# Optimization experiments

Measured on AMD Instinct MI355X. Metric: run time of the kernel, lower is better.

Reference implementation:

```python
import jax, jax.numpy as jnp
import numpy as np

N, H, F, E, K = 4096, 512, 2048, 8, 2  # tokens, hidden, ffn(=4H), experts, top_k


def setup_inputs() -> dict:
    key = jax.random.key(0)
    ks = jax.random.split(key, 7)
    def w(k, shape, fan_in):
        return jax.random.normal(k, shape, dtype=jnp.float32) * (fan_in ** -0.5)
    return {
        "x": jax.random.normal(ks[0], (N, H), dtype=jnp.float32),
        "W_in": w(ks[1], (H, H), H),          # input_proj.weight  [out,in]
        "W_router": w(ks[2], (E, H), H),      # router.gate.weight [E,H]
        "W_gate": w(ks[3], (E, F, H), H),     # per-expert gate_proj.weight
        "W_up": w(ks[4], (E, F, H), H),       # per-expert up_proj.weight
        "W_down": w(ks[5], (E, H, F), F),     # per-expert down_proj.weight
        "W_out": w(ks[6], (H, H), H),         # output_proj.weight
    }


def reference(x, W_in, W_router, W_gate, W_up, W_down, W_out):
    h = x @ W_in.T                                  # [N,H] input_proj
    logits = h @ W_router.T                         # [N,E]
    # route_mode='balanced' and world_size==1 -> expert_bias is None
    probs = jax.nn.softmax(logits, axis=-1)
    top_w, top_i = jax.lax.top_k(probs, K)          # [N,K]
    top_w = jax.nn.softmax(top_w, axis=-1)          # renormalize over top-k

    # per-token combine weight for each expert: [N,E]
    onehot = jax.nn.one_hot(top_i, E, dtype=h.dtype)      # [N,K,E]
    combine_w = jnp.einsum('nk,nke->ne', top_w, onehot)

    def expert(wg, wu, wd):
        # SwiGLU FFN: down( silu(gate(h)) * up(h) )
        return (jax.nn.silu(h @ wg.T) * (h @ wu.T)) @ wd.T  # [N,H]

    expert_out = jax.vmap(expert)(W_gate, W_up, W_down)     # [E,N,H]
    combined = jnp.einsum('ne,enh->nh', combine_w, expert_out)
    return combined @ W_out.T                                # output_proj
```

## Files before the change

### kernel.cpp

```cpp
#include <hip/hip_runtime.h>

typedef unsigned short u16;
typedef unsigned int u32;
typedef short bf16x8 __attribute__((ext_vector_type(8)));
typedef float f32x4 __attribute__((ext_vector_type(4)));

#define AS1 __attribute__((address_space(1)))
#define AS3 __attribute__((address_space(3)))

#define NTOK 4096
#define HDIM 512
#define FDIM 2048
#define NEXP 8
#define NASSIGN (NTOK * 2)
#define NPAD (NASSIGN + NEXP * 128)
#define RBMAX 128

__device__ __forceinline__ void g2l16(const void* g, void* l) {
  __builtin_amdgcn_global_load_lds((const AS1 u32*)g, (AS3 u32*)l, 16, 0, 0);
}
__device__ __forceinline__ u16 f2bf(float f) {
  u32 u = __float_as_uint(f);
  u = (u + 0x7FFFu + ((u >> 16) & 1u)) >> 16;
  return (u16)u;
}
__device__ __forceinline__ float bf2f(u16 h) { return __uint_as_float(((u32)h) << 16); }

#define WAITV6() asm volatile("s_waitcnt vmcnt(6)" ::: "memory")
#define WAITV4() asm volatile("s_waitcnt vmcnt(4)" ::: "memory")
#define WAITV0() asm volatile("s_waitcnt vmcnt(0)" ::: "memory")
#define BAR() __builtin_amdgcn_s_barrier()
#define VMBAR() do { WAITV0(); BAR(); } while (0)

__global__ __launch_bounds__(256) void cvtall_kernel(
    const float* __restrict__ x, const float* __restrict__ Wi, const float* __restrict__ Wo,
    const float* __restrict__ Wg, const float* __restrict__ Wu, const float* __restrict__ Wd,
    u16* __restrict__ xb, u16* __restrict__ Wib, u16* __restrict__ Wob,
    u16* __restrict__ Wgb, u16* __restrict__ Wub, u16* __restrict__ Wdb) {
  const int gid = blockIdx.x * 256 + threadIdx.x;
  const int S = 6784 * 256;
#pragma unroll
  for (int k = 0; k < 4; ++k) {
    const int i = gid + k * S;
    const float* s; u16* d; int o;
    if (i < 524288) { s = x; d = xb; o = i; }
    else if (i < 589824) { s = Wi; d = Wib; o = i - 524288; }
    else if (i < 655360) { s = Wo; d = Wob; o = i - 589824; }
    else if (i < 2752512) { s = Wg; d = Wgb; o = i - 655360; }
    else if (i < 4849664) { s = Wu; d = Wub; o = i - 2752512; }
    else { s = Wd; d = Wdb; o = i - 4849664; }
    const float4 v = ((const float4*)s)[o];
    ushort4 t; t.x = f2bf(v.x); t.y = f2bf(v.y); t.z = f2bf(v.z); t.w = f2bf(v.w);
    ((ushort4*)d)[o] = t;
  }
}

__global__ __launch_bounds__(256) void wreff_kernel(
    const float* __restrict__ Wr, const float* __restrict__ Wi, double* __restrict__ wre) {
  const int t = blockIdx.x * 256 + threadIdx.x;
  const int e = t >> 9, k = t & 511;
  const float* wr = Wr + e * HDIM;
  double a = 0.0;
  for (int j = 0; j < HDIM; j += 8) {
#pragma unroll
    for (int u = 0; u < 8; ++u) a += (double)wr[j + u] * (double)Wi[(j + u) * HDIM + k];
  }
  wre[t] = a;
}

__global__ __launch_bounds__(256) void router_kernel(
    const float* __restrict__ x, const double* __restrict__ wre,
    int* __restrict__ idx, float* __restrict__ wts) {
  __shared__ double lw[NEXP * HDIM];
  for (int i = threadIdx.x; i < NEXP * HDIM; i += 256) lw[i] = wre[i];
  __syncthreads();
  const int n = blockIdx.x * 256 + threadIdx.x;
  const float* xr = x + (size_t)n * HDIM;
  double acc[NEXP] = {};
  for (int k4 = 0; k4 < HDIM / 4; ++k4) {
    const float4 xv = ((const float4*)xr)[k4];
    const float xc[4] = {xv.x, xv.y, xv.z, xv.w};
#pragma unroll
    for (int c = 0; c < 4; ++c) {
      const double xd = (double)xc[c];
#pragma unroll
      for (int e = 0; e < NEXP; ++e) acc[e] += xd * lw[e * HDIM + k4 * 4 + c];
    }
  }
  double mx = acc[0];
#pragma unroll
  for (int e = 1; e < NEXP; ++e) mx = acc[e] > mx ? acc[e] : mx;
  double p[NEXP], se = 0.0;
#pragma unroll
  for (int e = 0; e < NEXP; ++e) { p[e] = exp(acc[e] - mx); se += p[e]; }
  const double inv = 1.0 / se;
#pragma unroll
  for (int e = 0; e < NEXP; ++e) p[e] *= inv;
  int i0 = 0; double b0 = p[0];
#pragma unroll
  for (int e = 1; e < NEXP; ++e) if (p[e] > b0) { b0 = p[e]; i0 = e; }
  int i1 = -1; double b1 = -1.0;
#pragma unroll
  for (int e = 0; e < NEXP; ++e) if (e != i0 && p[e] > b1) { b1 = p[e]; i1 = e; }
  const double e0 = exp(b0), e1 = exp(b1);
  idx[2 * n] = i0; idx[2 * n + 1] = i1;
  wts[2 * n] = (float)(e0 / (e0 + e1));
  wts[2 * n + 1] = (float)(e1 / (e0 + e1));
}

__global__ void assign_kernel(const int* __restrict__ idx, int* __restrict__ tok,
                              int* __restrict__ pos, int* __restrict__ rbe,
                              int* __restrict__ rbp, int* __restrict__ nrb) {
  __shared__ int cnt[NEXP], cur[NEXP];
  const int tid = threadIdx.x;
  if (tid < NEXP) cnt[tid] = 0;
  __syncthreads();
  for (int a = tid; a < NASSIGN; a += 256) atomicAdd(&cnt[idx[a]], 1);
  __syncthreads();
  if (tid == 0) {
    int o = 0, n = 0;
    for (int e = 0; e < NEXP; ++e) {
      cur[e] = o;
      const int nb = (cnt[e] + 127) >> 7;
      for (int i = 0; i < nb; ++i) { rbe[n] = e; rbp[n] = o + i * 128; ++n; }
      o += nb * 128;
    }
    nrb[0] = n;
  }
  __syncthreads();
  for (int p = tid; p < NPAD; p += 256) tok[p] = 0;
  __syncthreads();
  for (int a = tid; a < NASSIGN; a += 256) {
    const int e = idx[a];
    const int q = atomicAdd(&cur[e], 1);
    tok[q] = a >> 1;
    pos[a] = q;
  }
}

template <int SB, int NT>
__device__ __forceinline__ void gemm128_body(
    const u16* __restrict__ A, const u16* __restrict__ B, void* __restrict__ C,
    int m0, int n0, int N, int K, u16* sm, int tid) {
  u16 *lA0 = sm, *lA1 = sm + 8192, *lB0 = sm + 16384, *lB1 = sm + 24576;
  const int w = tid >> 6, l = tid & 63;
  const int wm = (w >> 2) * 64, wn = (w & 3) * 32;
  const int lm = l & 15, lk = (l >> 4) * 8, xr = (l & 7) << 3;
  const int sr = l >> 3, sc = ((l & 7) ^ sr) * 8;
  const u16* As = A + (size_t)(m0 + w * 8 + sr) * K + sc;
  const u16* Bs = B + (size_t)(n0 + w * 8 + sr) * K + sc;
  f32x4 acc[4][2] = {};
  auto STG = [&](u16* dA, u16* dB, int kt) {
    g2l16(As + kt, dA + w * 512);
    g2l16(As + (size_t)64 * K + kt, dA + 4096 + w * 512);
    g2l16(Bs + kt, dB + w * 512);
    g2l16(Bs + (size_t)64 * K + kt, dB + 4096 + w * 512);
  };
  auto CMP = [&](const u16* a_, const u16* b_) {
#pragma unroll
    for (int kk = 0; kk < 2; ++kk) {
      const int ko = (kk * 32 + lk) ^ xr;
      bf16x8 af[4], bf[2];
#pragma unroll
      for (int i = 0; i < 4; ++i) af[i] = *(const bf16x8*)(a_ + (wm + i * 16 + lm) * 64 + ko);
#pragma unroll
      for (int j = 0; j < 2; ++j) bf[j] = *(const bf16x8*)(b_ + (wn + j * 16 + lm) * 64 + ko);
#pragma unroll
      for (int i = 0; i < 4; ++i)
#pragma unroll
        for (int j = 0; j < 2; ++j)
          acc[i][j] = __builtin_amdgcn_mfma_f32_16x16x32_bf16(af[i], bf[j], acc[i][j], 0, 0, 0);
    }
  };
  STG(lA0, lB0, 0);
  VMBAR();
  for (int t = 0; t < NT; t += 2) {
    if (t + 1 < NT) STG(lA1, lB1, (t + 1) * 64);
    CMP(lA0, lB0);
    VMBAR();
    if (t + 2 < NT) STG(lA0, lB0, (t + 2) * 64);
    CMP(lA1, lB1);
    VMBAR();
  }
  const int cr = (l >> 4) * 4, cc = lm;
#pragma unroll
  for (int i = 0; i < 4; ++i)
#pragma unroll
    for (int j = 0; j < 2; ++j)
#pragma unroll
      for (int r = 0; r < 4; ++r) {
        const size_t o = (size_t)(m0 + wm + i * 16 + cr + r) * N + n0 + wn + j * 16 + cc;
        if (SB) ((u16*)C)[o] = f2bf(acc[i][j][r]);
        else ((float*)C)[o] = acc[i][j][r];
      }
}

__global__ __launch_bounds__(512, 2) void ingemm_kernel(
    const u16* __restrict__ xb, const u16* __restrict__ Wib, u16* __restrict__ hb) {
  __shared__ __align__(16) u16 sm[32768];
  gemm128_body<1, 8>(xb, Wib, hb, blockIdx.y * 128, blockIdx.x * 128, HDIM, HDIM, sm, threadIdx.x);
}

__global__ __launch_bounds__(512, 2) void outgemm_kernel(
    const u16* __restrict__ cb, const u16* __restrict__ Wob, float* __restrict__ out) {
  __shared__ __align__(16) u16 sm[32768];
  gemm128_body<0, 8>(cb, Wob, out, blockIdx.y * 128, blockIdx.x * 128, HDIM, HDIM, sm, threadIdx.x);
}

__global__ __launch_bounds__(512, 2) void gateup_kernel(
    const u16* __restrict__ hb, const u16* __restrict__ Wg, const u16* __restrict__ Wu,
    u16* __restrict__ act, const int* __restrict__ tok, const int* __restrict__ rbe,
    const int* __restrict__ rbp, const int* __restrict__ nrb) {
  const int rb = blockIdx.y;
  if (rb >= nrb[0]) return;
  __shared__ __align__(16) u16 sm[73728];
  const int e = rbe[rb], p0 = rbp[rb], n0 = blockIdx.x * 128;
  const int tid = threadIdx.x, w = tid >> 6, l = tid & 63;
  const int wm = (w >> 2) * 64, wn = (w & 3) * 32;
  const int lm = l & 15, lk = (l >> 4) * 8, xr = (l & 7) << 3;
  const int sr = l >> 3, sc = ((l & 7) ^ sr) * 8;
  const u16* A0 = hb + (size_t)tok[p0 + w * 8 + sr] * HDIM + sc;
  const u16* A1 = hb + (size_t)tok[p0 + 64 + w * 8 + sr] * HDIM + sc;
  const u16* G0 = Wg + (size_t)e * FDIM * HDIM + (size_t)(n0 + w * 8 + sr) * HDIM + sc;
  const u16* G1 = G0 + (size_t)64 * HDIM;
  const u16* U0 = Wu + (size_t)e * FDIM * HDIM + (size_t)(n0 + w * 8 + sr) * HDIM + sc;
  const u16* U1 = U0 + (size_t)64 * HDIM;
  f32x4 ag[4][2] = {}, au[4][2] = {};
  auto STG = [&](int b, int kt) {
    u16* d = sm + b * 24576;
    g2l16(A0 + kt, d + w * 512);
    g2l16(A1 + kt, d + 4096 + w * 512);
    g2l16(G0 + kt, d + 8192 + w * 512);
    g2l16(G1 + kt, d + 12288 + w * 512);
    g2l16(U0 + kt, d + 16384 + w * 512);
    g2l16(U1 + kt, d + 20480 + w * 512);
  };
  auto CMP = [&](int b) {
    const u16* a_ = sm + b * 24576;
    const u16* g_ = a_ + 8192;
    const u16* u_ = a_ + 16384;
#pragma unroll
    for (int kk = 0; kk < 2; ++kk) {
      const int ko = (kk * 32 + lk) ^ xr;
      bf16x8 af[4], gf[2], uf[2];
#pragma unroll
      for (int i = 0; i < 4; ++i) af[i] = *(const bf16x8*)(a_ + (wm + i * 16 + lm) * 64 + ko);
#pragma unroll
      for (int j = 0; j < 2; ++j) {
        gf[j] = *(const bf16x8*)(g_ + (wn + j * 16 + lm) * 64 + ko);
        uf[j] = *(const bf16x8*)(u_ + (wn + j * 16 + lm) * 64 + ko);
      }
#pragma unroll
      for (int i = 0; i < 4; ++i)
#pragma unroll
        for (int j = 0; j < 2; ++j) {
          ag[i][j] = __builtin_amdgcn_mfma_f32_16x16x32_bf16(af[i], gf[j], ag[i][j], 0, 0, 0);
          au[i][j] = __builtin_amdgcn_mfma_f32_16x16x32_bf16(af[i], uf[j], au[i][j], 0, 0, 0);
        }
    }
  };
  STG(0, 0); STG(1, 64);
  WAITV6(); BAR();
#pragma unroll
  for (int t = 0; t < 8; ++t) {
    if (t + 2 < 8) STG((t + 2) % 3, (t + 2) * 64);
    CMP(t % 3);
    if (t + 2 < 8) WAITV6(); else WAITV0();
    BAR();
  }
  const int cr = (l >> 4) * 4, cc = lm;
#pragma unroll
  for (int i = 0; i < 4; ++i)
#pragma unroll
    for (int j = 0; j < 2; ++j)
#pragma unroll
      for (int r = 0; r < 4; ++r) {
        const float g = ag[i][j][r], u = au[i][j][r];
        const float s = g / (1.0f + __expf(-g));
        act[(size_t)(p0 + wm + i * 16 + cr + r) * FDIM + n0 + wn + j * 16 + cc] = f2bf(s * u);
      }
}

__global__ __launch_bounds__(512, 2) void down_kernel(
    const u16* __restrict__ act, const u16* __restrict__ Wd, u16* __restrict__ dwn,
    const int* __restrict__ rbe, const int* __restrict__ rbp, const int* __restrict__ nrb) {
  const int rb = blockIdx.y;
  if (rb >= nrb[0]) return;
  __shared__ __align__(16) u16 sm[49152];
  const int e = rbe[rb], p0 = rbp[rb], n0 = blockIdx.x * 128;
  const int tid = threadIdx.x, w = tid >> 6, l = tid & 63;
  const int g = w >> 2;
  const int wm = ((w >> 1) & 1) * 64, wn = (w & 1) * 64;
  const int lm = l & 15, lk = (l >> 4) * 8, xr = (l & 7) << 3;
  const int ko = (g * 32 + lk) ^ xr;
  const int sr = l >> 3, sc = ((l & 7) ^ sr) * 8;
  const u16* As = act + (size_t)(p0 + w * 8 + sr) * FDIM + sc;
  const u16* Bs = Wd + (size_t)e * HDIM * FDIM + (size_t)(n0 + w * 8 + sr) * FDIM + sc;
  f32x4 acc[4][4] = {};
  auto STG = [&](int b, int kt) {
    u16* d = sm + b * 16384;
    g2l16(As + kt, d + w * 512);
    g2l16(As + (size_t)64 * FDIM + kt, d + 4096 + w * 512);
    g2l16(Bs + kt, d + 8192 + w * 512);
    g2l16(Bs + (size_t)64 * FDIM + kt, d + 12288 + w * 512);
  };
  auto CMP = [&](int b) {
    const u16* a_ = sm + b * 16384;
    const u16* b_ = a_ + 8192;
    bf16x8 af[4], bf[4];
#pragma unroll
    for (int i = 0; i < 4; ++i) af[i] = *(const bf16x8*)(a_ + (wm + i * 16 + lm) * 64 + ko);
#pragma unroll
    for (int j = 0; j < 4; ++j) bf[j] = *(const bf16x8*)(b_ + (wn + j * 16 + lm) * 64 + ko);
#pragma unroll
    for (int i = 0; i < 4; ++i)
#pragma unroll
      for (int j = 0; j < 4; ++j)
        acc[i][j] = __builtin_amdgcn_mfma_f32_16x16x32_bf16(af[i], bf[j], acc[i][j], 0, 0, 0);
  };
  STG(0, 0); STG(1, 64);
  WAITV4(); BAR();
#pragma unroll
  for (int t = 0; t < 32; ++t) {
    if (t + 2 < 32) STG((t + 2) % 3, (t + 2) * 64);
    CMP(t % 3);
    if (t + 2 < 32) WAITV4(); else WAITV0();
    BAR();
  }
  asm volatile("s_waitcnt lgkmcnt(0)" ::: "memory");
  __builtin_amdgcn_sched_barrier(0);
  BAR();
  float* red = (float*)sm;
  if (g == 1) {
#pragma unroll
    for (int i = 0; i < 4; ++i)
#pragma unroll
      for (int j = 0; j < 4; ++j)
        *(f32x4*)&red[(w & 3) * 4096 + (i * 4 + j) * 256 + l * 4] = acc[i][j];
  }
  BAR();
  if (g == 0) {
    const int cr = (l >> 4) * 4, cc = lm;
#pragma unroll
    for (int i = 0; i < 4; ++i)
#pragma unroll
      for (int j = 0; j < 4; ++j) {
        const f32x4 o = *(const f32x4*)&red[w * 4096 + (i * 4 + j) * 256 + l * 4];
        const f32x4 s = acc[i][j] + o;
#pragma unroll
        for (int r = 0; r < 4; ++r)
          dwn[(size_t)(p0 + wm + i * 16 + cr + r) * HDIM + n0 + wn + j * 16 + cc] = f2bf(s[r]);
      }
  }
}

__global__ void combine_kernel(const u16* __restrict__ dwn, const int* __restrict__ pos,
                               const float* __restrict__ wts, u16* __restrict__ cb) {
  const int n = blockIdx.x, t = threadIdx.x;
  const int p0 = pos[2 * n], p1 = pos[2 * n + 1];
  const float w0 = wts[2 * n], w1 = wts[2 * n + 1];
  const ushort4 a = ((const ushort4*)(dwn + (size_t)p0 * HDIM))[t];
  const ushort4 b = ((const ushort4*)(dwn + (size_t)p1 * HDIM))[t];
  ushort4 o;
  o.x = f2bf(w0 * bf2f(a.x) + w1 * bf2f(b.x));
  o.y = f2bf(w0 * bf2f(a.y) + w1 * bf2f(b.y));
  o.z = f2bf(w0 * bf2f(a.z) + w1 * bf2f(b.z));
  o.w = f2bf(w0 * bf2f(a.w) + w1 * bf2f(b.w));
  ((ushort4*)(cb + (size_t)n * HDIM))[t] = o;
}

extern "C" void kernel_launch(void* const* d_in, const int* in_sizes, int n_in,
                              void* d_out, int out_size, void* d_ws, size_t ws_size,
                              hipStream_t stream) {
  const float* x  = (const float*)d_in[0];
  const float* Wi = (const float*)d_in[1];
  const float* Wr = (const float*)d_in[2];
  const float* Wg = (const float*)d_in[3];
  const float* Wu = (const float*)d_in[4];
  const float* Wd = (const float*)d_in[5];
  const float* Wo = (const float*)d_in[6];
  float* out = (float*)d_out;

  char* ws = (char*)d_ws;
  size_t off = 0;
  auto alloc = [&](size_t bytes) -> void* {
    off = (off + 255) & ~(size_t)255;
    void* p = ws + off;
    off += bytes;
    return p;
  };
  u16* xb  = (u16*)alloc((size_t)NTOK * HDIM * 2);
  u16* hb  = (u16*)alloc((size_t)NTOK * HDIM * 2);
  u16* cb  = (u16*)alloc((size_t)NTOK * HDIM * 2);
  u16* Wib = (u16*)alloc((size_t)HDIM * HDIM * 2);
  u16* Wob = (u16*)alloc((size_t)HDIM * HDIM * 2);
  u16* Wgb = (u16*)alloc((size_t)NEXP * FDIM * HDIM * 2);
  u16* Wub = (u16*)alloc((size_t)NEXP * FDIM * HDIM * 2);
  u16* Wdb = (u16*)alloc((size_t)NEXP * HDIM * FDIM * 2);
  u16* actb = (u16*)alloc((size_t)NPAD * FDIM * 2);
  u16* dwn = (u16*)alloc((size_t)NPAD * HDIM * 2);
  double* wre = (double*)alloc((size_t)NEXP * HDIM * 8);
  int* idx = (int*)alloc((size_t)NASSIGN * 4);
  float* wts = (float*)alloc((size_t)NASSIGN * 4);
  int* tok = (int*)alloc((size_t)NPAD * 4);
  int* pos = (int*)alloc((size_t)NASSIGN * 4);
  int* rbe = (int*)alloc((size_t)RBMAX * 4);
  int* rbp = (int*)alloc((size_t)RBMAX * 4);
  int* nrb = (int*)alloc(256);

  cvtall_kernel<<<6784, 256, 0, stream>>>(x, Wi, Wo, Wg, Wu, Wd, xb, Wib, Wob, Wgb, Wub, Wdb);
  wreff_kernel<<<16, 256, 0, stream>>>(Wr, Wi, wre);
  router_kernel<<<16, 256, 0, stream>>>(x, wre, idx, wts);
  assign_kernel<<<1, 256, 0, stream>>>(idx, tok, pos, rbe, rbp, nrb);
  ingemm_kernel<<<dim3(4, 32), 512, 0, stream>>>(xb, Wib, hb);
  gateup_kernel<<<dim3(16, 72), 512, 0, stream>>>(hb, Wgb, Wub, actb, tok, rbe, rbp, nrb);
  down_kernel<<<dim3(4, 72), 512, 0, stream>>>(actb, Wdb, dwn, rbe, rbp, nrb);
  combine_kernel<<<NTOK, 128, 0, stream>>>(dwn, pos, wts, cb);
  outgemm_kernel<<<dim3(4, 32), 512, 0, stream>>>(cb, Wob, out);
}
```

Before: 218.2 us.

## Retile MoE gate/up to 256-row blocks, simplify down GEMM, fuse router-weight prep

Result: slower. 226.7 us (+3.9%).

```diff
diff --git a/kernel.cpp b/kernel.cpp
--- a/kernel.cpp
+++ b/kernel.cpp
@@ -13,7 +13,7 @@
 #define FDIM 2048
 #define NEXP 8
 #define NASSIGN (NTOK * 2)
-#define NPAD (NASSIGN + NEXP * 128)
+#define NPAD2 (NASSIGN + NEXP * 256)
 #define RBMAX 128
 
 __device__ __forceinline__ void g2l16(const void* g, void* l) {
@@ -26,7 +26,6 @@
 }
 __device__ __forceinline__ float bf2f(u16 h) { return __uint_as_float(((u32)h) << 16); }
 
-#define WAITV6() asm volatile("s_waitcnt vmcnt(6)" ::: "memory")
 #define WAITV4() asm volatile("s_waitcnt vmcnt(4)" ::: "memory")
 #define WAITV0() asm volatile("s_waitcnt vmcnt(0)" ::: "memory")
 #define BAR() __builtin_amdgcn_s_barrier()
@@ -35,46 +34,48 @@
 __global__ __launch_bounds__(256) void cvtall_kernel(
     const float* __restrict__ x, const float* __restrict__ Wi, const float* __restrict__ Wo,
     const float* __restrict__ Wg, const float* __restrict__ Wu, const float* __restrict__ Wd,
+    const float* __restrict__ Wr,
     u16* __restrict__ xb, u16* __restrict__ Wib, u16* __restrict__ Wob,
-    u16* __restrict__ Wgb, u16* __restrict__ Wub, u16* __restrict__ Wdb) {
-  const int gid = blockIdx.x * 256 + threadIdx.x;
-  const int S = 6784 * 256;
-#pragma unroll
-  for (int k = 0; k < 4; ++k) {
-    const int i = gid + k * S;
-    const float* s; u16* d; int o;
-    if (i < 524288) { s = x; d = xb; o = i; }
-    else if (i < 589824) { s = Wi; d = Wib; o = i - 524288; }
-    else if (i < 655360) { s = Wo; d = Wob; o = i - 589824; }
-    else if (i < 2752512) { s = Wg; d = Wgb; o = i - 655360; }
-    else if (i < 4849664) { s = Wu; d = Wub; o = i - 2752512; }
-    else { s = Wd; d = Wdb; o = i - 4849664; }
-    const float4 v = ((const float4*)s)[o];
-    ushort4 t; t.x = f2bf(v.x); t.y = f2bf(v.y); t.z = f2bf(v.z); t.w = f2bf(v.w);
-    ((ushort4*)d)[o] = t;
-  }
-}
-
-__global__ __launch_bounds__(256) void wreff_kernel(
-    const float* __restrict__ Wr, const float* __restrict__ Wi, double* __restrict__ wre) {
-  const int t = blockIdx.x * 256 + threadIdx.x;
-  const int e = t >> 9, k = t & 511;
-  const float* wr = Wr + e * HDIM;
-  double a = 0.0;
-  for (int j = 0; j < HDIM; j += 8) {
-#pragma unroll
-    for (int u = 0; u < 8; ++u) a += (double)wr[j + u] * (double)Wi[(j + u) * HDIM + k];
-  }
-  wre[t] = a;
-}
-
-__global__ __launch_bounds__(256) void router_kernel(
+    u16* __restrict__ Wgb, u16* __restrict__ Wub, u16* __restrict__ Wdb,
+    double* __restrict__ wre) {
+  const int b = blockIdx.x, tid = threadIdx.x;
+  if (b < 6784) {
+    const int gid = b * 256 + tid;
+    const int S = 6784 * 256;
+#pragma unroll
+    for (int k = 0; k < 4; ++k) {
+      const int i = gid + k * S;
+      const float* s; u16* d; int o;
+      if (i < 524288) { s = x; d = xb; o = i; }
+      else if (i < 589824) { s = Wi; d = Wib; o = i - 524288; }
+      else if (i < 655360) { s = Wo; d = Wob; o = i - 589824; }
+      else if (i < 2752512) { s = Wg; d = Wgb; o = i - 655360; }
+      else if (i < 4849664) { s = Wu; d = Wub; o = i - 2752512; }
+      else { s = Wd; d = Wdb; o = i - 4849664; }
+      const float4 v = ((const float4*)s)[o];
+      ushort4 t; t.x = f2bf(v.x); t.y = f2bf(v.y); t.z = f2bf(v.z); t.w = f2bf(v.w);
+      ((ushort4*)d)[o] = t;
+    }
+  } else {
+    const int t = (b - 6784) * 256 + tid;
+    const int e = t >> 9, k = t & 511;
+    const float* wr = Wr + e * HDIM;
+    double a = 0.0;
+    for (int j = 0; j < HDIM; j += 8) {
+#pragma unroll
+      for (int u = 0; u < 8; ++u) a += (double)wr[j + u] * (double)Wi[(j + u) * HDIM + k];
+    }
+    wre[t] = a;
+  }
+}
+
+__global__ __launch_bounds__(128) void router_kernel(
     const float* __restrict__ x, const double* __restrict__ wre,
     int* __restrict__ idx, float* __restrict__ wts) {
   __shared__ double lw[NEXP * HDIM];
-  for (int i = threadIdx.x; i < NEXP * HDIM; i += 256) lw[i] = wre[i];
+  for (int i = threadIdx.x; i < NEXP * HDIM; i += 128) lw[i] = wre[i];
   __syncthreads();
-  const int n = blockIdx.x * 256 + threadIdx.x;
+  const int n = blockIdx.x * 128 + threadIdx.x;
   const float* xr = x + (size_t)n * HDIM;
   double acc[NEXP] = {};
   for (int k4 = 0; k4 < HDIM / 4; ++k4) {
@@ -109,8 +110,9 @@
 }
 
 __global__ void assign_kernel(const int* __restrict__ idx, int* __restrict__ tok,
-                              int* __restrict__ pos, int* __restrict__ rbe,
-                              int* __restrict__ rbp, int* __restrict__ nrb) {
+                              int* __restrict__ pos, int* __restrict__ rbe2,
+                              int* __restrict__ rbp2, int* __restrict__ rbe1,
+                              int* __restrict__ rbp1, int* __restrict__ nrb) {
   __shared__ int cnt[NEXP], cur[NEXP];
   const int tid = threadIdx.x;
   if (tid < NEXP) cnt[tid] = 0;
@@ -118,17 +120,19 @@
   for (int a = tid; a < NASSIGN; a += 256) atomicAdd(&cnt[idx[a]], 1);
   __syncthreads();
   if (tid == 0) {
-    int o = 0, n = 0;
+    int o = 0, n2 = 0, n1 = 0;
     for (int e = 0; e < NEXP; ++e) {
       cur[e] = o;
-      const int nb = (cnt[e] + 127) >> 7;
-      for (int i = 0; i < nb; ++i) { rbe[n] = e; rbp[n] = o + i * 128; ++n; }
-      o += nb * 128;
-    }
-    nrb[0] = n;
+      const int nb2 = (cnt[e] + 255) >> 8;
+      const int nb1 = (cnt[e] + 127) >> 7;
+      for (int i = 0; i < nb2; ++i) { rbe2[n2] = e; rbp2[n2] = o + i * 256; ++n2; }
+      for (int i = 0; i < nb1; ++i) { rbe1[n1] = e; rbp1[n1] = o + i * 128; ++n1; }
+      o += nb2 * 256;
+    }
+    nrb[0] = n2; nrb[1] = n1;
   }
   __syncthreads();
-  for (int p = tid; p < NPAD; p += 256) tok[p] = 0;
+  for (int p = tid; p < NPAD2; p += 256) tok[p] = 0;
   __syncthreads();
   for (int a = tid; a < NASSIGN; a += 256) {
     const int e = idx[a];
@@ -209,149 +213,130 @@
 
 __global__ __launch_bounds__(512, 2) void gateup_kernel(
     const u16* __restrict__ hb, const u16* __restrict__ Wg, const u16* __restrict__ Wu,
-    u16* __restrict__ act, const int* __restrict__ tok, const int* __restrict__ rbe,
-    const int* __restrict__ rbp, const int* __restrict__ nrb) {
+    u16* __restrict__ act, const int* __restrict__ tok, const int* __restrict__ rbe2,
+    const int* __restrict__ rbp2, const int* __restrict__ nrb) {
   const int rb = blockIdx.y;
   if (rb >= nrb[0]) return;
-  __shared__ __align__(16) u16 sm[73728];
-  const int e = rbe[rb], p0 = rbp[rb], n0 = blockIdx.x * 128;
+  __shared__ __align__(16) u16 sm[49152];
+  const int e = rbe2[rb], p0 = rbp2[rb], n0 = blockIdx.x * 128;
   const int tid = threadIdx.x, w = tid >> 6, l = tid & 63;
-  const int wm = (w >> 2) * 64, wn = (w & 3) * 32;
-  const int lm = l & 15, lk = (l >> 4) * 8, xr = (l & 7) << 3;
-  const int sr = l >> 3, sc = ((l & 7) ^ sr) * 8;
-  const u16* A0 = hb + (size_t)tok[p0 + w * 8 + sr] * HDIM + sc;
-  const u16* A1 = hb + (size_t)tok[p0 + 64 + w * 8 + sr] * HDIM + sc;
-  const u16* G0 = Wg + (size_t)e * FDIM * HDIM + (size_t)(n0 + w * 8 + sr) * HDIM + sc;
-  const u16* G1 = G0 + (size_t)64 * HDIM;
-  const u16* U0 = Wu + (size_t)e * FDIM * HDIM + (size_t)(n0 + w * 8 + sr) * HDIM + sc;
-  const u16* U1 = U0 + (size_t)64 * HDIM;
-  f32x4 ag[4][2] = {}, au[4][2] = {};
-  auto STG = [&](int b, int kt) {
-    u16* d = sm + b * 24576;
-    g2l16(A0 + kt, d + w * 512);
-    g2l16(A1 + kt, d + 4096 + w * 512);
-    g2l16(G0 + kt, d + 8192 + w * 512);
-    g2l16(G1 + kt, d + 12288 + w * 512);
-    g2l16(U0 + kt, d + 16384 + w * 512);
-    g2l16(U1 + kt, d + 20480 + w * 512);
+  const int lrow = l >> 2;
+  const int scb = ((l & 3) ^ ((lrow >> 1) & 3)) * 8;
+  const int rm = (w >> 2) * 128, cg = (w & 3) * 32;
+  const int lm = l & 15;
+  const int koe = ((l >> 4) ^ ((l >> 1) & 3)) << 3;
+  const u16* As0 = hb + (size_t)tok[p0 + (w * 2 + 0) * 16 + lrow] * HDIM + scb;
+  const u16* As1 = hb + (size_t)tok[p0 + (w * 2 + 1) * 16 + lrow] * HDIM + scb;
+  const u16* Gs = Wg + (size_t)e * FDIM * HDIM + (size_t)(n0 + w * 16 + lrow) * HDIM + scb;
+  const u16* Us = Wu + (size_t)e * FDIM * HDIM + (size_t)(n0 + w * 16 + lrow) * HDIM + scb;
+  f32x4 ag[8][2] = {}, au[8][2] = {};
+  auto STG = [&](int b, int t) {
+    u16* base = sm + b * 16384;
+    const int kt = t * 32;
+    g2l16(As0 + kt, base + (w * 2 + 0) * 512);
+    g2l16(As1 + kt, base + (w * 2 + 1) * 512);
+    g2l16(Gs + kt, base + 8192 + w * 512);
+    g2l16(Us + kt, base + 12288 + w * 512);
   };
   auto CMP = [&](int b) {
-    const u16* a_ = sm + b * 24576;
+    const u16* a_ = sm + b * 16384;
     const u16* g_ = a_ + 8192;
-    const u16* u_ = a_ + 16384;
-#pragma unroll
-    for (int kk = 0; kk < 2; ++kk) {
-      const int ko = (kk * 32 + lk) ^ xr;
-      bf16x8 af[4], gf[2], uf[2];
-#pragma unroll
-      for (int i = 0; i < 4; ++i) af[i] = *(const bf16x8*)(a_ + (wm + i * 16 + lm) * 64 + ko);
+    const u16* u_ = a_ + 12288;
+    bf16x8 gf[2], uf[2];
+#pragma unroll
+    for (int j = 0; j < 2; ++j) {
+      gf[j] = *(const bf16x8*)(g_ + (cg + j * 16 + lm) * 32 + koe);
+      uf[j] = *(const bf16x8*)(u_ + (cg + j * 16 + lm) * 32 + koe);
+    }
+#pragma unroll
+    for (int i = 0; i < 8; ++i) {
+      const bf16x8 af = *(const bf16x8*)(a_ + (rm + i * 16 + lm) * 32 + koe);
 #pragma unroll
       for (int j = 0; j < 2; ++j) {
-        gf[j] = *(const bf16x8*)(g_ + (wn + j * 16 + lm) * 64 + ko);
-        uf[j] = *(const bf16x8*)(u_ + (wn + j * 16 + lm) * 64 + ko);
+        ag[i][j] = __builtin_amdgcn_mfma_f32_16x16x32_bf16(af, gf[j], ag[i][j], 0, 0, 0);
+        au[i][j] = __builtin_amdgcn_mfma_f32_16x16x32_bf16(af, uf[j], au[i][j], 0, 0, 0);
       }
-#pragma unroll
-      for (int i = 0; i < 4; ++i)
-#pragma unroll
-        for (int j = 0; j < 2; ++j) {
-          ag[i][j] = __builtin_amdgcn_mfma_f32_16x16x32_bf16(af[i], gf[j], ag[i][j], 0, 0, 0);
-          au[i][j] = __builtin_amdgcn_mfma_f32_16x16x32_bf16(af[i], uf[j], au[i][j], 0, 0, 0);
-        }
-    }
-  };
-  STG(0, 0); STG(1, 64);
-  WAITV6(); BAR();
-#pragma unroll
-  for (int t = 0; t < 8; ++t) {
-    if (t + 2 < 8) STG((t + 2) % 3, (t + 2) * 64);
+    }
+  };
+  STG(0, 0); STG(1, 1);
+  WAITV4(); BAR();
+#pragma unroll
+  for (int t = 0; t < 16; ++t) {
+    if (t + 2 < 16) STG((t + 2) % 3, t + 2);
     CMP(t % 3);
-    if (t + 2 < 8) WAITV6(); else WAITV0();
+    if (t + 2 < 16) { WAITV4(); } else { WAITV0(); }
     BAR();
   }
   const int cr = (l >> 4) * 4, cc = lm;
 #pragma unroll
-  for (int i = 0; i < 4; ++i)
+  for (int i = 0; i < 8; ++i)
 #pragma unroll
     for (int j = 0; j < 2; ++j)
 #pragma unroll
       for (int r = 0; r < 4; ++r) {
         const float g = ag[i][j][r], u = au[i][j][r];
         const float s = g / (1.0f + __expf(-g));
-        act[(size_t)(p0 + wm + i * 16 + cr + r) * FDIM + n0 + wn + j * 16 + cc] = f2bf(s * u);
+        act[(size_t)(p0 + rm + i * 16 + cr + r) * FDIM + n0 + cg + j * 16 + cc] = f2bf(s * u);
       }
 }
 
-__global__ __launch_bounds__(512, 2) void down_kernel(
+__global__ __launch_bounds__(256, 3) void down_kernel(
     const u16* __restrict__ act, const u16* __restrict__ Wd, u16* __restrict__ dwn,
-    const int* __restrict__ rbe, const int* __restrict__ rbp, const int* __restrict__ nrb) {
+    const int* __restrict__ rbe1, const int* __restrict__ rbp1, const int* __restrict__ nrb) {
   const int rb = blockIdx.y;
-  if (rb >= nrb[0]) return;
-  __shared__ __align__(16) u16 sm[49152];
-  const int e = rbe[rb], p0 = rbp[rb], n0 = blockIdx.x * 128;
+  if (rb >= nrb[1]) return;
+  __shared__ __align__(16) u16 sm[24576];
+  const int e = rbe1[rb], p0 = rbp1[rb], n0 = blockIdx.x * 128;
   const int tid = threadIdx.x, w = tid >> 6, l = tid & 63;
-  const int g = w >> 2;
-  const int wm = ((w >> 1) & 1) * 64, wn = (w & 1) * 64;
-  const int lm = l & 15, lk = (l >> 4) * 8, xr = (l & 7) << 3;
-  const int ko = (g * 32 + lk) ^ xr;
-  const int sr = l >> 3, sc = ((l & 7) ^ sr) * 8;
-  const u16* As = act + (size_t)(p0 + w * 8 + sr) * FDIM + sc;
-  const u16* Bs = Wd + (size_t)e * HDIM * FDIM + (size_t)(n0 + w * 8 + sr) * FDIM + sc;
+  const int lrow = l >> 2;
+  const int scb = ((l & 3) ^ ((lrow >> 1) & 3)) * 8;
+  const int wm = (w >> 1) * 64, wn = (w & 1) * 64;
+  const int lm = l & 15;
+  const int koe = ((l >> 4) ^ ((l >> 1) & 3)) << 3;
+  const u16* As0 = act + (size_t)(p0 + (w * 2 + 0) * 16 + lrow) * FDIM + scb;
+  const u16* As1 = act + (size_t)(p0 + (w * 2 + 1) * 16 + lrow) * FDIM + scb;
+  const u16* Bs0 = Wd + (size_t)e * HDIM * FDIM + (size_t)(n0 + (w * 2 + 0) * 16 + lrow) * FDIM + scb;
+  const u16* Bs1 = Wd + (size_t)e * HDIM * FDIM + (size_t)(n0 + (w * 2 + 1) * 16 + lrow) * FDIM + scb;
   f32x4 acc[4][4] = {};
-  auto STG = [&](int b, int kt) {
-    u16* d = sm + b * 16384;
-    g2l16(As + kt, d + w * 512);
-    g2l16(As + (size_t)64 * FDIM + kt, d + 4096 + w * 512);
-    g2l16(Bs + kt, d + 8192 + w * 512);
-    g2l16(Bs + (size_t)64 * FDIM + kt, d + 12288 + w * 512);
+  auto STG = [&](int b, int t) {
+    u16* base = sm + b * 8192;
+    const int kt = t * 32;
+    g2l16(As0 + kt, base + (w * 2 + 0) * 512);
+    g2l16(As1 + kt, base + (w * 2 + 1) * 512);
+    g2l16(Bs0 + kt, base + 4096 + (w * 2 + 0) * 512);
+    g2l16(Bs1 + kt, base + 4096 + (w * 2 + 1) * 512);
   };
   auto CMP = [&](int b) {
-    const u16* a_ = sm + b * 16384;
-    const u16* b_ = a_ + 8192;
-    bf16x8 af[4], bf[4];
-#pragma unroll
-    for (int i = 0; i < 4; ++i) af[i] = *(const bf16x8*)(a_ + (wm + i * 16 + lm) * 64 + ko);
-#pragma unroll
-    for (int j = 0; j < 4; ++j) bf[j] = *(const bf16x8*)(b_ + (wn + j * 16 + lm) * 64 + ko);
-#pragma unroll
-    for (int i = 0; i < 4; ++i)
+    const u16* a_ = sm + b * 8192;
+    const u16* b_ = a_ + 4096;
+    bf16x8 bf[4];
+#pragma unroll
+    for (int j = 0; j < 4; ++j) bf[j] = *(const bf16x8*)(b_ + (wn + j * 16 + lm) * 32 + koe);
+#pragma unroll
+    for (int i = 0; i < 4; ++i) {
+      const bf16x8 af = *(const bf16x8*)(a_ + (wm + i * 16 + lm) * 32 + koe);
 #pragma unroll
       for (int j = 0; j < 4; ++j)
-        acc[i][j] = __builtin_amdgcn_mfma_f32_16x16x32_bf16(af[i], bf[j], acc[i][j], 0, 0, 0);
-  };
-  STG(0, 0); STG(1, 64);
+        acc[i][j] = __builtin_amdgcn_mfma_f32_16x16x32_bf16(af, bf[j], acc[i][j], 0, 0, 0);
+    }
+  };
+  STG(0, 0); STG(1, 1);
   WAITV4(); BAR();
 #pragma unroll
-  for (int t = 0; t < 32; ++t) {
-    if (t + 2 < 32) STG((t + 2) % 3, (t + 2) * 64);
+  for (int t = 0; t < 64; ++t) {
+    if (t + 2 < 64) STG((t + 2) % 3, t + 2);
     CMP(t % 3);
-    if (t + 2 < 32) WAITV4(); else WAITV0();
+    if (t + 2 < 64) { WAITV4(); } else { WAITV0(); }
     BAR();
   }
-  asm volatile("s_waitcnt lgkmcnt(0)" ::: "memory");
-  __builtin_amdgcn_sched_barrier(0);
-  BAR();
-  float* red = (float*)sm;
-  if (g == 1) {
-#pragma unroll
-    for (int i = 0; i < 4; ++i)
-#pragma unroll
-      for (int j = 0; j < 4; ++j)
-        *(f32x4*)&red[(w & 3) * 4096 + (i * 4 + j) * 256 + l * 4] = acc[i][j];
-  }
-  BAR();
-  if (g == 0) {
-    const int cr = (l >> 4) * 4, cc = lm;
-#pragma unroll
-    for (int i = 0; i < 4; ++i)
-#pragma unroll
-      for (int j = 0; j < 4; ++j) {
-        const f32x4 o = *(const f32x4*)&red[w * 4096 + (i * 4 + j) * 256 + l * 4];
-        const f32x4 s = acc[i][j] + o;
-#pragma unroll
-        for (int r = 0; r < 4; ++r)
-          dwn[(size_t)(p0 + wm + i * 16 + cr + r) * HDIM + n0 + wn + j * 16 + cc] = f2bf(s[r]);
-      }
-  }
+  const int cr = (l >> 4) * 4, cc = lm;
+#pragma unroll
+  for (int i = 0; i < 4; ++i)
+#pragma unroll
+    for (int j = 0; j < 4; ++j)
+#pragma unroll
+      for (int r = 0; r < 4; ++r)
+        dwn[(size_t)(p0 + wm + i * 16 + cr + r) * HDIM + n0 + wn + j * 16 + cc] = f2bf(acc[i][j][r]);
 }
 
 __global__ void combine_kernel(const u16* __restrict__ dwn, const int* __restrict__ pos,
@@ -397,24 +382,26 @@
   u16* Wgb = (u16*)alloc((size_t)NEXP * FDIM * HDIM * 2);
   u16* Wub = (u16*)alloc((size_t)NEXP * FDIM * HDIM * 2);
   u16* Wdb = (u16*)alloc((size_t)NEXP * HDIM * FDIM * 2);
-  u16* actb = (u16*)alloc((size_t)NPAD * FDIM * 2);
-  u16* dwn = (u16*)alloc((size_t)NPAD * HDIM * 2);
+  u16* actb = (u16*)alloc((size_t)NPAD2 * FDIM * 2);
+  u16* dwn = (u16*)alloc((size_t)NPAD2 * HDIM * 2);
   double* wre = (double*)alloc((size_t)NEXP * HDIM * 8);
   int* idx = (int*)alloc((size_t)NASSIGN * 4);
   float* wts = (float*)alloc((size_t)NASSIGN * 4);
-  int* tok = (int*)alloc((size_t)NPAD * 4);
+  int* tok = (int*)alloc((size_t)NPAD2 * 4);
   int* pos = (int*)alloc((size_t)NASSIGN * 4);
-  int* rbe = (int*)alloc((size_t)RBMAX * 4);
-  int* rbp = (int*)alloc((size_t)RBMAX * 4);
+  int* rbe2 = (int*)alloc((size_t)RBMAX * 4);
+  int* rbp2 = (int*)alloc((size_t)RBMAX * 4);
+  int* rbe1 = (int*)alloc((size_t)RBMAX * 4);
+  int* rbp1 = (int*)alloc((size_t)RBMAX * 4);
   int* nrb = (int*)alloc(256);
 
-  cvtall_kernel<<<6784, 256, 0, stream>>>(x, Wi, Wo, Wg, Wu, Wd, xb, Wib, Wob, Wgb, Wub, Wdb);
-  wreff_kernel<<<16, 256, 0, stream>>>(Wr, Wi, wre);
-  router_kernel<<<16, 256, 0, stream>>>(x, wre, idx, wts);
-  assign_kernel<<<1, 256, 0, stream>>>(idx, tok, pos, rbe, rbp, nrb);
+  cvtall_kernel<<<6800, 256, 0, stream>>>(x, Wi, Wo, Wg, Wu, Wd, Wr,
+                                          xb, Wib, Wob, Wgb, Wub, Wdb, wre);
+  router_kernel<<<32, 128, 0, stream>>>(x, wre, idx, wts);
+  assign_kernel<<<1, 256, 0, stream>>>(idx, tok, pos, rbe2, rbp2, rbe1, rbp1, nrb);
   ingemm_kernel<<<dim3(4, 32), 512, 0, stream>>>(xb, Wib, hb);
-  gateup_kernel<<<dim3(16, 72), 512, 0, stream>>>(hb, Wgb, Wub, actb, tok, rbe, rbp, nrb);
-  down_kernel<<<dim3(4, 72), 512, 0, stream>>>(actb, Wdb, dwn, rbe, rbp, nrb);
+  gateup_kernel<<<dim3(16, 40), 512, 0, stream>>>(hb, Wgb, Wub, actb, tok, rbe2, rbp2, nrb);
+  down_kernel<<<dim3(4, 72), 256, 0, stream>>>(actb, Wdb, dwn, rbe1, rbp1, nrb);
   combine_kernel<<<NTOK, 128, 0, stream>>>(dwn, pos, wts, cb);
   outgemm_kernel<<<dim3(4, 32), 512, 0, stream>>>(cb, Wob, out);
 }
```

## Fuse fp32-to-bf16 conversion of x, W_in, W_out into projection GEMMs

Applied to the files above, without the earlier changes.

Measured after the change: 233.3 us. 6.9% more time.

```diff
diff --git a/kernel.cpp b/kernel.cpp
--- a/kernel.cpp
+++ b/kernel.cpp
@@ -1,4 +1,5 @@
 #include <hip/hip_runtime.h>
+#include <hip/hip_bf16.h>
 
 typedef unsigned short u16;
 typedef unsigned int u32;
@@ -25,34 +26,54 @@
   return (u16)u;
 }
 __device__ __forceinline__ float bf2f(u16 h) { return __uint_as_float(((u32)h) << 16); }
+__device__ __forceinline__ u32 pkbf(float a, float b) {
+  __hip_bfloat162 h = __float22bfloat162_rn(float2{a, b});
+  u32 r;
+  __builtin_memcpy(&r, &h, 4);
+  return r;
+}
+__device__ __forceinline__ int4 pk8(const float4 a, const float4 b) {
+  int4 r;
+  r.x = (int)pkbf(a.x, a.y); r.y = (int)pkbf(a.z, a.w);
+  r.z = (int)pkbf(b.x, b.y); r.w = (int)pkbf(b.z, b.w);
+  return r;
+}
 
 #define WAITV6() asm volatile("s_waitcnt vmcnt(6)" ::: "memory")
 #define WAITV4() asm volatile("s_waitcnt vmcnt(4)" ::: "memory")
+#define WAITV2() asm volatile("s_waitcnt vmcnt(2)" ::: "memory")
 #define WAITV0() asm volatile("s_waitcnt vmcnt(0)" ::: "memory")
+#define LGKM0() asm volatile("s_waitcnt lgkmcnt(0)" ::: "memory")
 #define BAR() __builtin_amdgcn_s_barrier()
+#define SCB() __builtin_amdgcn_sched_barrier(0)
+#define PRIO1() __builtin_amdgcn_s_setprio(1)
+#define PRIO0() __builtin_amdgcn_s_setprio(0)
 #define VMBAR() do { WAITV0(); BAR(); } while (0)
 
-__global__ __launch_bounds__(256) void cvtall_kernel(
-    const float* __restrict__ x, const float* __restrict__ Wi, const float* __restrict__ Wo,
+__global__ __launch_bounds__(256) void cvtw_kernel(
     const float* __restrict__ Wg, const float* __restrict__ Wu, const float* __restrict__ Wd,
-    u16* __restrict__ xb, u16* __restrict__ Wib, u16* __restrict__ Wob,
     u16* __restrict__ Wgb, u16* __restrict__ Wub, u16* __restrict__ Wdb) {
   const int gid = blockIdx.x * 256 + threadIdx.x;
-  const int S = 6784 * 256;
-#pragma unroll
-  for (int k = 0; k < 4; ++k) {
-    const int i = gid + k * S;
-    const float* s; u16* d; int o;
-    if (i < 524288) { s = x; d = xb; o = i; }
-    else if (i < 589824) { s = Wi; d = Wib; o = i - 524288; }
-    else if (i < 655360) { s = Wo; d = Wob; o = i - 589824; }
-    else if (i < 2752512) { s = Wg; d = Wgb; o = i - 655360; }
-    else if (i < 4849664) { s = Wu; d = Wub; o = i - 2752512; }
-    else { s = Wd; d = Wdb; o = i - 4849664; }
-    const float4 v = ((const float4*)s)[o];
-    ushort4 t; t.x = f2bf(v.x); t.y = f2bf(v.y); t.z = f2bf(v.z); t.w = f2bf(v.w);
-    ((ushort4*)d)[o] = t;
-  }
+  const float* sp[6];
+  u16* dp[6];
+#pragma unroll
+  for (int i = 0; i < 6; ++i) {
+    const int p = gid + i * 524288;
+    const int seg = p >> 20;
+    const size_t off = (size_t)(p & 1048575) * 8;
+    const float* s = (seg == 0) ? Wg : (seg == 1) ? Wu : Wd;
+    u16* d = (seg == 0) ? Wgb : (seg == 1) ? Wub : Wdb;
+    sp[i] = s + off;
+    dp[i] = d + off;
+  }
+  float4 a[12];
+#pragma unroll
+  for (int i = 0; i < 6; ++i) {
+    a[2 * i] = ((const float4*)sp[i])[0];
+    a[2 * i + 1] = ((const float4*)sp[i])[1];
+  }
+#pragma unroll
+  for (int i = 0; i < 6; ++i) *(int4*)dp[i] = pk8(a[2 * i], a[2 * i + 1]);
 }
 
 __global__ __launch_bounds__(256) void wreff_kernel(
@@ -60,21 +81,23 @@
   const int t = blockIdx.x * 256 + threadIdx.x;
   const int e = t >> 9, k = t & 511;
   const float* wr = Wr + e * HDIM;
-  double a = 0.0;
-  for (int j = 0; j < HDIM; j += 8) {
-#pragma unroll
-    for (int u = 0; u < 8; ++u) a += (double)wr[j + u] * (double)Wi[(j + u) * HDIM + k];
-  }
-  wre[t] = a;
-}
-
-__global__ __launch_bounds__(256) void router_kernel(
+  double a0 = 0.0, a1 = 0.0, a2 = 0.0, a3 = 0.0;
+  for (int j = 0; j < HDIM; j += 4) {
+    a0 += (double)wr[j + 0] * (double)Wi[(j + 0) * HDIM + k];
+    a1 += (double)wr[j + 1] * (double)Wi[(j + 1) * HDIM + k];
+    a2 += (double)wr[j + 2] * (double)Wi[(j + 2) * HDIM + k];
+    a3 += (double)wr[j + 3] * (double)Wi[(j + 3) * HDIM + k];
+  }
+  wre[t] = (a0 + a1) + (a2 + a3);
+}
+
+__global__ __launch_bounds__(128) void router_kernel(
     const float* __restrict__ x, const double* __restrict__ wre,
     int* __restrict__ idx, float* __restrict__ wts) {
   __shared__ double lw[NEXP * HDIM];
-  for (int i = threadIdx.x; i < NEXP * HDIM; i += 256) lw[i] = wre[i];
+  for (int i = threadIdx.x; i < NEXP * HDIM; i += 128) lw[i] = wre[i];
   __syncthreads();
-  const int n = blockIdx.x * 256 + threadIdx.x;
+  const int n = blockIdx.x * 128 + threadIdx.x;
   const float* xr = x + (size_t)n * HDIM;
   double acc[NEXP] = {};
   for (int k4 = 0; k4 < HDIM / 4; ++k4) {
@@ -138,49 +161,60 @@
   }
 }
 
-template <int SB, int NT>
-__device__ __forceinline__ void gemm128_body(
-    const u16* __restrict__ A, const u16* __restrict__ B, void* __restrict__ C,
-    int m0, int n0, int N, int K, u16* sm, int tid) {
-  u16 *lA0 = sm, *lA1 = sm + 8192, *lB0 = sm + 16384, *lB1 = sm + 24576;
-  const int w = tid >> 6, l = tid & 63;
+__global__ __launch_bounds__(512, 2) void ingemm_kernel(
+    const float* __restrict__ x, const float* __restrict__ Wi, u16* __restrict__ hb) {
+  __shared__ __align__(16) u16 sm[32768];
+  const int m0 = blockIdx.y * 128, n0 = blockIdx.x * 128;
+  const int tid = threadIdx.x, w = tid >> 6, l = tid & 63;
   const int wm = (w >> 2) * 64, wn = (w & 3) * 32;
-  const int lm = l & 15, lk = (l >> 4) * 8, xr = (l & 7) << 3;
-  const int sr = l >> 3, sc = ((l & 7) ^ sr) * 8;
-  const u16* As = A + (size_t)(m0 + w * 8 + sr) * K + sc;
-  const u16* Bs = B + (size_t)(n0 + w * 8 + sr) * K + sc;
+  const int lm = l & 15, lk = (l >> 4) * 8, xr = (l & 7) * 8;
+  const int lr = l >> 3, c8 = l & 7;
+  const int ko0 = lk ^ xr, ko1 = (32 + lk) ^ xr;
+  const int wcol = (c8 ^ lr) * 8;
+  const float* Ap0 = x + (size_t)(m0 + w * 8 + lr) * HDIM + c8 * 8;
+  const float* Ap1 = Ap0 + (size_t)64 * HDIM;
+  const float* Bp0 = Wi + (size_t)(n0 + w * 8 + lr) * HDIM + c8 * 8;
+  const float* Bp1 = Bp0 + (size_t)64 * HDIM;
   f32x4 acc[4][2] = {};
-  auto STG = [&](u16* dA, u16* dB, int kt) {
-    g2l16(As + kt, dA + w * 512);
-    g2l16(As + (size_t)64 * K + kt, dA + 4096 + w * 512);
-    g2l16(Bs + kt, dB + w * 512);
-    g2l16(Bs + (size_t)64 * K + kt, dB + 4096 + w * 512);
-  };
-  auto CMP = [&](const u16* a_, const u16* b_) {
+  float4 v0, v1, v2, v3, v4, v5, v6, v7;
+  auto WLOAD = [&](int kt) {
+    v0 = *(const float4*)(Ap0 + kt); v1 = *(const float4*)(Ap0 + kt + 4);
+    v2 = *(const float4*)(Ap1 + kt); v3 = *(const float4*)(Ap1 + kt + 4);
+    v4 = *(const float4*)(Bp0 + kt); v5 = *(const float4*)(Bp0 + kt + 4);
+    v6 = *(const float4*)(Bp1 + kt); v7 = *(const float4*)(Bp1 + kt + 4);
+  };
+  auto WWRITE = [&](u16* st) {
+    *(int4*)(st + (w * 8 + lr) * 64 + wcol) = pk8(v0, v1);
+    *(int4*)(st + (64 + w * 8 + lr) * 64 + wcol) = pk8(v2, v3);
+    *(int4*)(st + 8192 + (w * 8 + lr) * 64 + wcol) = pk8(v4, v5);
+    *(int4*)(st + 8192 + (64 + w * 8 + lr) * 64 + wcol) = pk8(v6, v7);
+  };
+  WLOAD(0);
+  WAITV0(); WWRITE(sm);
+  LGKM0(); BAR(); SCB();
+  for (int t = 0; t < 8; ++t) {
+    u16* bu = sm + (t & 1) * 16384;
+    u16* bn = sm + ((t + 1) & 1) * 16384;
+    if (t < 7) WLOAD((t + 1) * 64);
+    const u16 *a_ = bu, *b_ = bu + 8192;
 #pragma unroll
     for (int kk = 0; kk < 2; ++kk) {
-      const int ko = (kk * 32 + lk) ^ xr;
+      const int ko = kk ? ko1 : ko0;
       bf16x8 af[4], bf[2];
 #pragma unroll
       for (int i = 0; i < 4; ++i) af[i] = *(const bf16x8*)(a_ + (wm + i * 16 + lm) * 64 + ko);
 #pragma unroll
       for (int j = 0; j < 2; ++j) bf[j] = *(const bf16x8*)(b_ + (wn + j * 16 + lm) * 64 + ko);
+      PRIO1();
 #pragma unroll
       for (int i = 0; i < 4; ++i)
 #pragma unroll
         for (int j = 0; j < 2; ++j)
           acc[i][j] = __builtin_amdgcn_mfma_f32_16x16x32_bf16(af[i], bf[j], acc[i][j], 0, 0, 0);
+      PRIO0();
     }
-  };
-  STG(lA0, lB0, 0);
-  VMBAR();
-  for (int t = 0; t < NT; t += 2) {
-    if (t + 1 < NT) STG(lA1, lB1, (t + 1) * 64);
-    CMP(lA0, lB0);
-    VMBAR();
-    if (t + 2 < NT) STG(lA0, lB0, (t + 2) * 64);
-    CMP(lA1, lB1);
-    VMBAR();
+    if (t < 7) { WAITV0(); WWRITE(bn); }
+    LGKM0(); BAR(); SCB();
   }
   const int cr = (l >> 4) * 4, cc = lm;
 #pragma unroll
@@ -188,23 +222,74 @@
 #pragma unroll
     for (int j = 0; j < 2; ++j)
 #pragma unroll
-      for (int r = 0; r < 4; ++r) {
-        const size_t o = (size_t)(m0 + wm + i * 16 + cr + r) * N + n0 + wn + j * 16 + cc;
-        if (SB) ((u16*)C)[o] = f2bf(acc[i][j][r]);
-        else ((float*)C)[o] = acc[i][j][r];
-      }
-}
-
-__global__ __launch_bounds__(512, 2) void ingemm_kernel(
-    const u16* __restrict__ xb, const u16* __restrict__ Wib, u16* __restrict__ hb) {
+      for (int r = 0; r < 4; ++r)
+        hb[(size_t)(m0 + wm + i * 16 + cr + r) * HDIM + n0 + wn + j * 16 + cc] =
+            f2bf(acc[i][j][r]);
+}
+
+__global__ __launch_bounds__(512, 2) void outgemm_kernel(
+    const u16* __restrict__ cb, const float* __restrict__ Wo, float* __restrict__ out) {
   __shared__ __align__(16) u16 sm[32768];
-  gemm128_body<1, 8>(xb, Wib, hb, blockIdx.y * 128, blockIdx.x * 128, HDIM, HDIM, sm, threadIdx.x);
-}
-
-__global__ __launch_bounds__(512, 2) void outgemm_kernel(
-    const u16* __restrict__ cb, const u16* __restrict__ Wob, float* __restrict__ out) {
-  __shared__ __align__(16) u16 sm[32768];
-  gemm128_body<0, 8>(cb, Wob, out, blockIdx.y * 128, blockIdx.x * 128, HDIM, HDIM, sm, threadIdx.x);
+  const int m0 = blockIdx.y * 128, n0 = blockIdx.x * 128;
+  const int tid = threadIdx.x, w = tid >> 6, l = tid & 63;
+  const int wm = (w >> 2) * 64, wn = (w & 3) * 32;
+  const int lm = l & 15, lk = (l >> 4) * 8, xr = (l & 7) * 8;
+  const int lr = l >> 3, c8 = l & 7;
+  const int ko0 = lk ^ xr, ko1 = (32 + lk) ^ xr;
+  const int wcol = (c8 ^ lr) * 8;
+  const u16* Ap0 = cb + (size_t)(m0 + w * 8 + lr) * HDIM + wcol;
+  const u16* Ap1 = Ap0 + (size_t)64 * HDIM;
+  const float* Bp0 = Wo + (size_t)(n0 + w * 8 + lr) * HDIM + c8 * 8;
+  const float* Bp1 = Bp0 + (size_t)64 * HDIM;
+  f32x4 acc[4][2] = {};
+  float4 v4, v5, v6, v7;
+  auto WLOADB = [&](int kt) {
+    v4 = *(const float4*)(Bp0 + kt); v5 = *(const float4*)(Bp0 + kt + 4);
+    v6 = *(const float4*)(Bp1 + kt); v7 = *(const float4*)(Bp1 + kt + 4);
+  };
+  auto WWRITEB = [&](u16* st) {
+    *(int4*)(st + 8192 + (w * 8 + lr) * 64 + wcol) = pk8(v4, v5);
+    *(int4*)(st + 8192 + (64 + w * 8 + lr) * 64 + wcol) = pk8(v6, v7);
+  };
+  auto STGA = [&](u16* st, int kt) {
+    g2l16(Ap0 + kt, st + w * 512);
+    g2l16(Ap1 + kt, st + 4096 + w * 512);
+  };
+  WLOADB(0); SCB(); STGA(sm, 0);
+  WAITV2(); WWRITEB(sm);
+  WAITV0(); LGKM0(); BAR(); SCB();
+  for (int t = 0; t < 8; ++t) {
+    u16* bu = sm + (t & 1) * 16384;
+    u16* bn = sm + ((t + 1) & 1) * 16384;
+    if (t < 7) { WLOADB((t + 1) * 64); SCB(); STGA(bn, (t + 1) * 64); }
+    const u16 *a_ = bu, *b_ = bu + 8192;
+#pragma unroll
+    for (int kk = 0; kk < 2; ++kk) {
+      const int ko = kk ? ko1 : ko0;
+      bf16x8 af[4], bf[2];
+#pragma unroll
+      for (int i = 0; i < 4; ++i) af[i] = *(const bf16x8*)(a_ + (wm + i * 16 + lm) * 64 + ko);
+#pragma unroll
+      for (int j = 0; j < 2; ++j) bf[j] = *(const bf16x8*)(b_ + (wn + j * 16 + lm) * 64 + ko);
+      PRIO1();
+#pragma unroll
+      for (int i = 0; i < 4; ++i)
+#pragma unroll
+        for (int j = 0; j < 2; ++j)
+          acc[i][j] = __builtin_amdgcn_mfma_f32_16x16x32_bf16(af[i], bf[j], acc[i][j], 0, 0, 0);
+      PRIO0();
+    }
+    if (t < 7) { WAITV2(); WWRITEB(bn); WAITV0(); }
+    LGKM0(); BAR(); SCB();
+  }
+  const int cr = (l >> 4) * 4, cc = lm;
+#pragma unroll
+  for (int i = 0; i < 4; ++i)
+#pragma unroll
+    for (int j = 0; j < 2; ++j)
+#pragma unroll
+      for (int r = 0; r < 4; ++r)
+        out[(size_t)(m0 + wm + i * 16 + cr + r) * HDIM + n0 + wn + j * 16 + cc] = acc[i][j][r];
 }
 
 __global__ __launch_bounds__(512, 2) void gateup_kernel(
@@ -327,8 +412,8 @@
     if (t + 2 < 32) WAITV4(); else WAITV0();
     BAR();
   }
-  asm volatile("s_waitcnt lgkmcnt(0)" ::: "memory");
-  __builtin_amdgcn_sched_barrier(0);
+  LGKM0();
+  SCB();
   BAR();
   float* red = (float*)sm;
   if (g == 1) {
@@ -389,16 +474,13 @@
     off += bytes;
     return p;
   };
-  u16* xb  = (u16*)alloc((size_t)NTOK * HDIM * 2);
-  u16* hb  = (u16*)alloc((size_t)NTOK * HDIM * 2);
-  u16* cb  = (u16*)alloc((size_t)NTOK * HDIM * 2);
-  u16* Wib = (u16*)alloc((size_t)HDIM * HDIM * 2);
-  u16* Wob = (u16*)alloc((size_t)HDIM * HDIM * 2);
-  u16* Wgb = (u16*)alloc((size_t)NEXP * FDIM * HDIM * 2);
-  u16* Wub = (u16*)alloc((size_t)NEXP * FDIM * HDIM * 2);
-  u16* Wdb = (u16*)alloc((size_t)NEXP * HDIM * FDIM * 2);
+  u16* hb   = (u16*)alloc((size_t)NTOK * HDIM * 2);
+  u16* cb   = (u16*)alloc((size_t)NTOK * HDIM * 2);
+  u16* Wgb  = (u16*)alloc((size_t)NEXP * FDIM * HDIM * 2);
+  u16* Wub  = (u16*)alloc((size_t)NEXP * FDIM * HDIM * 2);
+  u16* Wdb  = (u16*)alloc((size_t)NEXP * HDIM * FDIM * 2);
   u16* actb = (u16*)alloc((size_t)NPAD * FDIM * 2);
-  u16* dwn = (u16*)alloc((size_t)NPAD * HDIM * 2);
+  u16* dwn  = (u16*)alloc((size_t)NPAD * HDIM * 2);
   double* wre = (double*)alloc((size_t)NEXP * HDIM * 8);
   int* idx = (int*)alloc((size_t)NASSIGN * 4);
   float* wts = (float*)alloc((size_t)NASSIGN * 4);
@@ -408,13 +490,13 @@
   int* rbp = (int*)alloc((size_t)RBMAX * 4);
   int* nrb = (int*)alloc(256);
 
-  cvtall_kernel<<<6784, 256, 0, stream>>>(x, Wi, Wo, Wg, Wu, Wd, xb, Wib, Wob, Wgb, Wub, Wdb);
+  cvtw_kernel<<<2048, 256, 0, stream>>>(Wg, Wu, Wd, Wgb, Wub, Wdb);
   wreff_kernel<<<16, 256, 0, stream>>>(Wr, Wi, wre);
-  router_kernel<<<16, 256, 0, stream>>>(x, wre, idx, wts);
+  router_kernel<<<32, 128, 0, stream>>>(x, wre, idx, wts);
   assign_kernel<<<1, 256, 0, stream>>>(idx, tok, pos, rbe, rbp, nrb);
-  ingemm_kernel<<<dim3(4, 32), 512, 0, stream>>>(xb, Wib, hb);
+  ingemm_kernel<<<dim3(4, 32), 512, 0, stream>>>(x, Wi, hb);
   gateup_kernel<<<dim3(16, 72), 512, 0, stream>>>(hb, Wgb, Wub, actb, tok, rbe, rbp, nrb);
   down_kernel<<<dim3(4, 72), 512, 0, stream>>>(actb, Wdb, dwn, rbe, rbp, nrb);
   combine_kernel<<<NTOK, 128, 0, stream>>>(dwn, pos, wts, cb);
-  outgemm_kernel<<<dim3(4, 32), 512, 0, stream>>>(cb, Wob, out);
-}
+  outgemm_kernel<<<dim3(4, 32), 512, 0, stream>>>(cb, Wo, out);
+}
```
